# Optimization experiments

Measured on AMD Instinct MI355X. Metric: run time of the kernel, lower is better.

## Reference

```python
import jax, jax.numpy as jnp
import numpy as np

B, D, N, K = 4, 256, 4096, 8192


def setup_inputs() -> dict:
    key = jax.random.key(0)
    kx, ke = jax.random.split(key)
    x = jax.random.normal(kx, (B, D, N), dtype=jnp.float32)
    e = jax.random.normal(ke, (K, D), dtype=jnp.float32)
    return {"x": x, "e": e}


def reference(x, e):
    # encode: cdist(x^T [B,N,D], e [K,D]) -> [B,N,K]; argmin over K.
    # sqrt is monotonic, so argmin of squared distance == argmin of cdist.
    xt = jnp.transpose(x, (0, 2, 1))                      # [B,N,D]
    x2 = jnp.sum(xt * xt, axis=-1, keepdims=True)         # [B,N,1]
    e2 = jnp.sum(e * e, axis=-1)                          # [K]
    d2 = x2 - 2.0 * jnp.einsum('bnd,kd->bnk', xt, e) + e2 # [B,N,K]
    codes = jnp.argmin(d2, axis=-1)                       # [B,N]
    # decode: embedding gather then transpose back to [B,D,N]
    quantized = e[codes]                                  # [B,N,D]
    return jnp.transpose(quantized, (0, 2, 1))            # [B,D,N]
```

## Files before the change

kernel.cpp:

```cpp
#include <hip/hip_runtime.h>
#include <stdint.h>

#define B_ 4
#define D_ 256
#define N_ 4096
#define K_ 8192
#define Q_ (B_*N_)

#define KSPLIT_ 4
#define KSLICE_ (K_/KSPLIT_)
#define CHUNK_ 64
#define NCHUNK_ (KSLICE_/CHUNK_)
#define QTILE_ 256

typedef __attribute__((ext_vector_type(8))) short bf16x8;
typedef __attribute__((ext_vector_type(16))) float f32x16;

__device__ __forceinline__ unsigned short f32_to_bf16(float f) {
  unsigned u = __float_as_uint(f);
  unsigned r = 0x7FFFu + ((u >> 16) & 1u);
  return (unsigned short)((u + r) >> 16);
}
__device__ __forceinline__ float bf16_to_f32(unsigned short h) {
  return __uint_as_float(((unsigned)h) << 16);
}

__device__ __forceinline__ void gl_lds16(const void* g, void* l) {
  __builtin_amdgcn_global_load_lds(
      (const __attribute__((address_space(1))) unsigned int*)g,
      (__attribute__((address_space(3))) unsigned int*)l, 16, 0, 0);
}

__global__ void prep_x_kernel(const float* __restrict__ x,
                              unsigned short* __restrict__ xh,
                              unsigned short* __restrict__ xl) {
  __shared__ float tile[32][33];
  int b = blockIdx.z;
  int d0 = blockIdx.y * 32;
  int n0 = blockIdx.x * 32;
  int tx = threadIdx.x, ty = threadIdx.y;
  const float* xp = x + ((size_t)b * D_ + d0) * N_ + n0;
#pragma unroll
  for (int i = 0; i < 4; ++i)
    tile[ty + 8 * i][tx] = xp[(size_t)(ty + 8 * i) * N_ + tx];
  __syncthreads();
#pragma unroll
  for (int i = 0; i < 4; ++i) {
    int nl = ty + 8 * i;
    float v = tile[tx][nl];
    unsigned short h = f32_to_bf16(v);
    unsigned short l = f32_to_bf16(v - bf16_to_f32(h));
    size_t q = (size_t)b * N_ + n0 + nl;
    xh[q * D_ + d0 + tx] = h;
    xl[q * D_ + d0 + tx] = l;
  }
}

__global__ void prep_e_kernel(const float* __restrict__ e,
                              unsigned short* __restrict__ eh,
                              unsigned short* __restrict__ el,
                              float* __restrict__ e2h,
                              unsigned long long* __restrict__ keys) {
  int k = blockIdx.x;
  int d = threadIdx.x;
  if (d < 2) keys[(size_t)k * 2 + d] = ~0ull;
  float v = e[(size_t)k * D_ + d];
  unsigned short h = f32_to_bf16(v);
  unsigned short l = f32_to_bf16(v - bf16_to_f32(h));
  eh[(size_t)k * D_ + d] = h;
  el[(size_t)k * D_ + d] = l;
  float s = v * v;
#pragma unroll
  for (int off = 32; off > 0; off >>= 1) s += __shfl_down(s, off, 64);
  __shared__ float ws4[4];
  if ((threadIdx.x & 63) == 0) ws4[threadIdx.x >> 6] = s;
  __syncthreads();
  if (threadIdx.x == 0) e2h[k] = 0.5f * (ws4[0] + ws4[1] + ws4[2] + ws4[3]);
}

__global__ __launch_bounds__(512, 2) void vq_main_kernel(
    const unsigned short* __restrict__ xh, const unsigned short* __restrict__ xl,
    const unsigned short* __restrict__ eh, const unsigned short* __restrict__ el,
    const float* __restrict__ e2h, unsigned long long* __restrict__ keys) {
  __shared__ __attribute__((aligned(16))) unsigned short Bs[2][2][CHUNK_ * 256];

  const int tid = threadIdx.x;
  const int w = tid >> 6;
  const int lane = tid & 63;
  const int l = lane & 31;
  const int hi = lane >> 5;

  const int qt = blockIdx.x >> 2;
  const int ksl = blockIdx.x & 3;
  const int q0 = qt * QTILE_;
  const int kbase = ksl * KSLICE_;
  const int qw = q0 + w * 32;

  bf16x8 ah[16], al[16];
  {
    const unsigned short* pa = xh + (size_t)(qw + l) * D_ + hi * 8;
    const unsigned short* pb = xl + (size_t)(qw + l) * D_ + hi * 8;
#pragma unroll
    for (int kc16 = 0; kc16 < 16; ++kc16) {
      ah[kc16] = *(const bf16x8*)(pa + kc16 * 16);
      al[kc16] = *(const bf16x8*)(pb + kc16 * 16);
    }
  }

  float rminv[16];
  unsigned rmp[4];
#pragma unroll
  for (int r = 0; r < 16; ++r) rminv[r] = __builtin_inff();
#pragma unroll
  for (int i = 0; i < 4; ++i) rmp[i] = 0u;

  auto stage = [&](int ch, int buf) {
    const int kc = kbase + ch * CHUNK_;
#pragma unroll
    for (int p = 0; p < 4; ++p) {
      const int c0 = w * 8 + p * 2;
      const int c = c0 + hi;
      const int g = l ^ (c & 31);
      const size_t srcoff = (size_t)(kc + c) * D_ + g * 8;
      gl_lds16(eh + srcoff, &Bs[buf][0][c0 * 256]);
      gl_lds16(el + srcoff, &Bs[buf][1][c0 * 256]);
    }
  };

  stage(0, 0);

#pragma unroll 1
  for (int ch = 0; ch < NCHUNK_; ++ch) {
    const int buf = ch & 1;
    __syncthreads();
    if (ch + 1 < NCHUNK_) stage(ch + 1, buf ^ 1);
    const int kc = kbase + ch * CHUNK_;
    const float e2v0 = e2h[kc + l];
    const float e2v1 = e2h[kc + 32 + l];

    const unsigned short* bh_base = &Bs[buf][0][0];
    const unsigned short* bl_base = &Bs[buf][1][0];
#define RD(base, kk) \
    (*(const bf16x8*)&(base)[(((kk) >> 4) * 32 + l) * 256 + \
                             (((((kk) & 15) * 2 + hi) ^ l) * 8)])

    f32x16 acc0, acc1;
#pragma unroll
    for (int r = 0; r < 16; ++r) { acc0[r] = 0.f; acc1[r] = 0.f; }

    bf16x8 cbh = RD(bh_base, 0), cbl = RD(bl_base, 0);
    bf16x8 nbh = RD(bh_base, 1), nbl = RD(bl_base, 1);
#pragma unroll
    for (int kk = 0; kk < 32; ++kk) {
      const bf16x8 ubh = cbh, ubl = cbl;
      cbh = nbh; cbl = nbl;
      if (kk + 2 < 32) { nbh = RD(bh_base, kk + 2); nbl = RD(bl_base, kk + 2); }
      const int ks = kk & 15;
      if (kk < 16) {
        acc0 = __builtin_amdgcn_mfma_f32_32x32x16_bf16(ah[ks], ubh, acc0, 0, 0, 0);
        acc0 = __builtin_amdgcn_mfma_f32_32x32x16_bf16(ah[ks], ubl, acc0, 0, 0, 0);
        acc0 = __builtin_amdgcn_mfma_f32_32x32x16_bf16(al[ks], ubh, acc0, 0, 0, 0);
      } else {
        acc1 = __builtin_amdgcn_mfma_f32_32x32x16_bf16(ah[ks], ubh, acc1, 0, 0, 0);
        acc1 = __builtin_amdgcn_mfma_f32_32x32x16_bf16(ah[ks], ubl, acc1, 0, 0, 0);
        acc1 = __builtin_amdgcn_mfma_f32_32x32x16_bf16(al[ks], ubh, acc1, 0, 0, 0);
      }
      if (kk == 15) {
        const unsigned vc = (unsigned)(ch * 2 + 0);
#pragma unroll
        for (int r = 0; r < 16; ++r) {
          float dv = e2v0 - acc0[r];
          bool better = dv < rminv[r];
          rminv[r] = better ? dv : rminv[r];
          const unsigned sh = (r & 3) * 8;
          unsigned np = (rmp[r >> 2] & ~(0xFFu << sh)) | (vc << sh);
          rmp[r >> 2] = better ? np : rmp[r >> 2];
        }
      }
    }
#undef RD
    {
      const unsigned vc = (unsigned)(ch * 2 + 1);
#pragma unroll
      for (int r = 0; r < 16; ++r) {
        float dv = e2v1 - acc1[r];
        bool better = dv < rminv[r];
        rminv[r] = better ? dv : rminv[r];
        const unsigned sh = (r & 3) * 8;
        unsigned np = (rmp[r >> 2] & ~(0xFFu << sh)) | (vc << sh);
        rmp[r >> 2] = better ? np : rmp[r >> 2];
      }
    }
  }

#pragma unroll
  for (int r = 0; r < 16; ++r) {
    float bv = rminv[r];
    const unsigned sh = (r & 3) * 8;
    int bi = kbase + (int)((rmp[r >> 2] >> sh) & 0xFFu) * 32 + l;
#pragma unroll
    for (int xm = 1; xm <= 16; xm <<= 1) {
      float ov = __shfl_xor(bv, xm, 64);
      int oi = __shfl_xor(bi, xm, 64);
      if (ov < bv || (ov == bv && oi < bi)) { bv = ov; bi = oi; }
    }
    if (l == 0) {
      const int m = (r & 3) + 8 * (r >> 2) + 4 * hi;
      const int qq = qw + m;
      unsigned su = __float_as_uint(bv);
      su ^= (unsigned)(((int)su >> 31) | 0x80000000u);
      unsigned long long key = ((unsigned long long)su << 32) | (unsigned)bi;
      atomicMin(keys + qq, key);
    }
  }
}

__global__ void decode_kernel(const unsigned long long* __restrict__ keys,
                              const float* __restrict__ e,
                              float* __restrict__ out) {
  __shared__ float tile[32][33];
  __shared__ int codes[32];
  int b = blockIdx.y;
  int n0 = blockIdx.x * 32;
  int tx = threadIdx.x, ty = threadIdx.y;
  if (ty == 0)
    codes[tx] = (int)(keys[(size_t)b * N_ + n0 + tx] & 0xFFFFFFFFull);
  __syncthreads();
#pragma unroll 1
  for (int d0 = 0; d0 < D_; d0 += 32) {
#pragma unroll
    for (int i = 0; i < 4; ++i) {
      int nl = ty + 8 * i;
      tile[nl][tx] = e[(size_t)codes[nl] * D_ + d0 + tx];
    }
    __syncthreads();
#pragma unroll
    for (int i = 0; i < 4; ++i) {
      int dl = ty + 8 * i;
      out[((size_t)b * D_ + d0 + dl) * N_ + n0 + tx] = tile[tx][dl];
    }
    __syncthreads();
  }
}

extern "C" void kernel_launch(void* const* d_in, const int* in_sizes, int n_in,
                              void* d_out, int out_size, void* d_ws, size_t ws_size,
                              hipStream_t stream) {
  const float* x = (const float*)d_in[0];
  const float* e = (const float*)d_in[1];
  float* out = (float*)d_out;

  char* wksp = (char*)d_ws;
  unsigned short* xh = (unsigned short*)wksp;
  unsigned short* xl = xh + (size_t)Q_ * D_;
  unsigned short* eh = xl + (size_t)Q_ * D_;
  unsigned short* el = eh + (size_t)K_ * D_;
  float* e2h = (float*)(el + (size_t)K_ * D_);
  unsigned long long* keys = (unsigned long long*)(e2h + K_);

  prep_x_kernel<<<dim3(N_ / 32, D_ / 32, B_), dim3(32, 8), 0, stream>>>(x, xh, xl);
  prep_e_kernel<<<K_, 256, 0, stream>>>(e, eh, el, e2h, keys);
  vq_main_kernel<<<(Q_ / QTILE_) * KSPLIT_, 512, 0, stream>>>(xh, xl, eh, el, e2h, keys);
  decode_kernel<<<dim3(N_ / 32, B_), dim3(32, 8), 0, stream>>>(keys, e, out);
}
```

Measured before the change: 257.1 us.

## Merge x/e prep kernels into one vectorized launch and vectorize decode gather

Combines the two preprocessing kernels (x transpose+bf16 split and e split+norm+key init) into a single 1280-block launch. Both paths now use float4 loads and 4-wide bf16 stores, and x is transposed through a 64x256 LDS tile. The decode kernel gathers full 256-wide codebook rows into LDS with float4 loads, then writes transposed output with float4 stores. This removes one launch and cuts the number of narrow memory transactions, at the cost of a large LDS footprint per block and possible LDS bank conflicts on the transposed reads.

```diff
diff --git a/kernel.cpp b/kernel.cpp
--- a/kernel.cpp
+++ b/kernel.cpp
@@ -15,6 +15,7 @@
 
 typedef __attribute__((ext_vector_type(8))) short bf16x8;
 typedef __attribute__((ext_vector_type(16))) float f32x16;
+typedef __attribute__((ext_vector_type(4))) unsigned short us4;
 
 __device__ __forceinline__ unsigned short f32_to_bf16(float f) {
   unsigned u = __float_as_uint(f);
@@ -31,51 +32,66 @@
       (__attribute__((address_space(3))) unsigned int*)l, 16, 0, 0);
 }
 
-__global__ void prep_x_kernel(const float* __restrict__ x,
-                              unsigned short* __restrict__ xh,
-                              unsigned short* __restrict__ xl) {
-  __shared__ float tile[32][33];
-  int b = blockIdx.z;
-  int d0 = blockIdx.y * 32;
-  int n0 = blockIdx.x * 32;
-  int tx = threadIdx.x, ty = threadIdx.y;
-  const float* xp = x + ((size_t)b * D_ + d0) * N_ + n0;
-#pragma unroll
-  for (int i = 0; i < 4; ++i)
-    tile[ty + 8 * i][tx] = xp[(size_t)(ty + 8 * i) * N_ + tx];
-  __syncthreads();
-#pragma unroll
-  for (int i = 0; i < 4; ++i) {
-    int nl = ty + 8 * i;
-    float v = tile[tx][nl];
-    unsigned short h = f32_to_bf16(v);
-    unsigned short l = f32_to_bf16(v - bf16_to_f32(h));
-    size_t q = (size_t)b * N_ + n0 + nl;
-    xh[q * D_ + d0 + tx] = h;
-    xl[q * D_ + d0 + tx] = l;
-  }
-}
-
-__global__ void prep_e_kernel(const float* __restrict__ e,
-                              unsigned short* __restrict__ eh,
-                              unsigned short* __restrict__ el,
-                              float* __restrict__ e2h,
-                              unsigned long long* __restrict__ keys) {
-  int k = blockIdx.x;
-  int d = threadIdx.x;
-  if (d < 2) keys[(size_t)k * 2 + d] = ~0ull;
-  float v = e[(size_t)k * D_ + d];
-  unsigned short h = f32_to_bf16(v);
-  unsigned short l = f32_to_bf16(v - bf16_to_f32(h));
-  eh[(size_t)k * D_ + d] = h;
-  el[(size_t)k * D_ + d] = l;
-  float s = v * v;
-#pragma unroll
-  for (int off = 32; off > 0; off >>= 1) s += __shfl_down(s, off, 64);
-  __shared__ float ws4[4];
-  if ((threadIdx.x & 63) == 0) ws4[threadIdx.x >> 6] = s;
-  __syncthreads();
-  if (threadIdx.x == 0) e2h[k] = 0.5f * (ws4[0] + ws4[1] + ws4[2] + ws4[3]);
+__global__ __launch_bounds__(512) void prep_kernel(
+    const float* __restrict__ x, const float* __restrict__ e,
+    unsigned short* __restrict__ xh, unsigned short* __restrict__ xl,
+    unsigned short* __restrict__ eh, unsigned short* __restrict__ el,
+    float* __restrict__ e2h, unsigned long long* __restrict__ keys) {
+  __shared__ float tile[64][260];
+  const int t = threadIdx.x;
+  const int w = t >> 6;
+  const int lam = t & 63;
+
+  if (blockIdx.x < 256) {
+    const int b = blockIdx.x >> 6;
+    const int n0 = (blockIdx.x & 63) << 6;
+#pragma unroll
+    for (int p = 0; p < 4; ++p) {
+      const int d = p * 64 + (t >> 3);
+      const int f4 = t & 7;
+      const float* src = x + (size_t)(b * D_ + d) * N_ + n0;
+      float4 v1 = *(const float4*)(src + f4 * 4);
+      float4 v2 = *(const float4*)(src + 32 + f4 * 4);
+      tile[f4 * 4 + 0][d] = v1.x; tile[f4 * 4 + 1][d] = v1.y;
+      tile[f4 * 4 + 2][d] = v1.z; tile[f4 * 4 + 3][d] = v1.w;
+      tile[32 + f4 * 4 + 0][d] = v2.x; tile[32 + f4 * 4 + 1][d] = v2.y;
+      tile[32 + f4 * 4 + 2][d] = v2.z; tile[32 + f4 * 4 + 3][d] = v2.w;
+    }
+    __syncthreads();
+#pragma unroll
+    for (int i = 0; i < 8; ++i) {
+      const int q = w * 8 + i;
+      float4 v = *(const float4*)&tile[q][lam * 4];
+      unsigned short h0 = f32_to_bf16(v.x), h1 = f32_to_bf16(v.y);
+      unsigned short h2 = f32_to_bf16(v.z), h3 = f32_to_bf16(v.w);
+      us4 hv = {h0, h1, h2, h3};
+      us4 lv = {f32_to_bf16(v.x - bf16_to_f32(h0)),
+                f32_to_bf16(v.y - bf16_to_f32(h1)),
+                f32_to_bf16(v.z - bf16_to_f32(h2)),
+                f32_to_bf16(v.w - bf16_to_f32(h3))};
+      const size_t qg = (size_t)b * N_ + n0 + q;
+      *(us4*)(xh + qg * D_ + lam * 4) = hv;
+      *(us4*)(xl + qg * D_ + lam * 4) = lv;
+    }
+  } else {
+    const int k0 = ((int)blockIdx.x - 256) * 8;
+    const int k = k0 + w;
+    float4 v = *(const float4*)(e + (size_t)k * D_ + lam * 4);
+    unsigned short h0 = f32_to_bf16(v.x), h1 = f32_to_bf16(v.y);
+    unsigned short h2 = f32_to_bf16(v.z), h3 = f32_to_bf16(v.w);
+    us4 hv = {h0, h1, h2, h3};
+    us4 lv = {f32_to_bf16(v.x - bf16_to_f32(h0)),
+              f32_to_bf16(v.y - bf16_to_f32(h1)),
+              f32_to_bf16(v.z - bf16_to_f32(h2)),
+              f32_to_bf16(v.w - bf16_to_f32(h3))};
+    *(us4*)(eh + (size_t)k * D_ + lam * 4) = hv;
+    *(us4*)(el + (size_t)k * D_ + lam * 4) = lv;
+    float sq = v.x * v.x + v.y * v.y + v.z * v.z + v.w * v.w;
+#pragma unroll
+    for (int xm = 1; xm <= 32; xm <<= 1) sq += __shfl_xor(sq, xm, 64);
+    if (lam == 0) e2h[k] = 0.5f * sq;
+    if (t < 16) keys[(size_t)k0 * 2 + t] = ~0ull;
+  }
 }
 
 __global__ __launch_bounds__(512, 2) void vq_main_kernel(
@@ -215,31 +231,31 @@
   }
 }
 
-__global__ void decode_kernel(const unsigned long long* __restrict__ keys,
-                              const float* __restrict__ e,
-                              float* __restrict__ out) {
-  __shared__ float tile[32][33];
+__global__ __launch_bounds__(256) void decode_kernel(
+    const unsigned long long* __restrict__ keys,
+    const float* __restrict__ e, float* __restrict__ out) {
+  __shared__ float tile[32][260];
   __shared__ int codes[32];
-  int b = blockIdx.y;
-  int n0 = blockIdx.x * 32;
-  int tx = threadIdx.x, ty = threadIdx.y;
-  if (ty == 0)
-    codes[tx] = (int)(keys[(size_t)b * N_ + n0 + tx] & 0xFFFFFFFFull);
+  const int t = threadIdx.x;
+  const int b = blockIdx.y;
+  const int n0 = blockIdx.x * 32;
+  const int w = t >> 6, lam = t & 63;
+  if (t < 32)
+    codes[t] = (int)(keys[(size_t)b * N_ + n0 + t] & 0xFFFFFFFFull);
   __syncthreads();
-#pragma unroll 1
-  for (int d0 = 0; d0 < D_; d0 += 32) {
-#pragma unroll
-    for (int i = 0; i < 4; ++i) {
-      int nl = ty + 8 * i;
-      tile[nl][tx] = e[(size_t)codes[nl] * D_ + d0 + tx];
-    }
-    __syncthreads();
-#pragma unroll
-    for (int i = 0; i < 4; ++i) {
-      int dl = ty + 8 * i;
-      out[((size_t)b * D_ + d0 + dl) * N_ + n0 + tx] = tile[tx][dl];
-    }
-    __syncthreads();
+#pragma unroll
+  for (int i = 0; i < 8; ++i) {
+    const int row = w * 8 + i;
+    float4 ev = *(const float4*)(e + (size_t)codes[row] * D_ + lam * 4);
+    *(float4*)&tile[row][lam * 4] = ev;
+  }
+  __syncthreads();
+#pragma unroll
+  for (int iter = 0; iter < 8; ++iter) {
+    const int d = iter * 32 + (t >> 3);
+    const int nc = (t & 7) * 4;
+    float4 ov = {tile[nc][d], tile[nc + 1][d], tile[nc + 2][d], tile[nc + 3][d]};
+    *(float4*)(out + (size_t)(b * D_ + d) * N_ + n0 + nc) = ov;
   }
 }
 
@@ -258,8 +274,7 @@
   float* e2h = (float*)(el + (size_t)K_ * D_);
   unsigned long long* keys = (unsigned long long*)(e2h + K_);
 
-  prep_x_kernel<<<dim3(N_ / 32, D_ / 32, B_), dim3(32, 8), 0, stream>>>(x, xh, xl);
-  prep_e_kernel<<<K_, 256, 0, stream>>>(e, eh, el, e2h, keys);
+  prep_kernel<<<1280, 512, 0, stream>>>(x, e, xh, xl, eh, el, e2h, keys);
   vq_main_kernel<<<(Q_ / QTILE_) * KSPLIT_, 512, 0, stream>>>(xh, xl, eh, el, e2h, keys);
-  decode_kernel<<<dim3(N_ / 32, B_), dim3(32, 8), 0, stream>>>(keys, e, out);
-}
+  decode_kernel<<<dim3(N_ / 32, B_), 256, 0, stream>>>(keys, e, out);
+}
```

New measurement: 247.7 us. -3.6%, faster.
